# Performance work log

Measured on AMD Instinct MI355X. Metric: run time of the kernel, lower is better.

The kernel has to match this reference:

```python
import jax, jax.numpy as jnp
import numpy as np

N, R, B, H, C, E = 4096, 8, 30, 64, 16, 131072


def setup_inputs() -> dict:
    key = jax.random.key(0)
    ks = jax.random.split(key, 11)
    s = 0.02  # small init scale for weights
    return {
        "x": jax.random.normal(ks[0], (N, N), jnp.float32),
        "edge_index": jax.random.randint(ks[1], (2, E), 0, N, jnp.int32),
        "edge_type": jax.random.randint(ks[2], (E,), 0, R, jnp.int32),
        "basis1": jax.random.normal(ks[3], (B, N, H), jnp.float32) * s,
        "att1": jax.random.normal(ks[4], (R, B), jnp.float32) * s,
        "root1": jax.random.normal(ks[5], (N, H), jnp.float32) * s,
        "bias1": jnp.zeros((H,), jnp.float32),
        "basis2": jax.random.normal(ks[6], (B, H, C), jnp.float32) * s,
        "att2": jax.random.normal(ks[7], (R, B), jnp.float32) * s,
        "root2": jax.random.normal(ks[8], (H, C), jnp.float32) * s,
        "bias2": jnp.zeros((C,), jnp.float32),
    }


def _rgcn_conv(x, src, dst, etype, deg_inv, basis, att, root, bias):
    # Basis-decomposed relation weights: W_r = sum_b att[r,b] * basis[b]
    W = jnp.einsum("rb,bio->rio", att, basis)            # [R, in, out]
    # Pre-transform every node by every relation weight (equivalent to
    # per-edge bmm(x_j, W[edge_type]) but avoids gathering [E, in] features).
    h = jnp.einsum("ni,rio->nro", x, W)                  # [N, R, out]
    msg = h[src, etype]                                  # [E, out] per-edge message
    agg = jax.ops.segment_sum(msg, dst, num_segments=N)  # scatter-add to dst
    agg = agg * deg_inv[:, None]                         # scatter-mean (aggr='mean')
    return agg + x @ root + bias                         # root/self transform + bias


def reference(x, edge_index, edge_type, basis1, att1, root1, bias1,
              basis2, att2, root2, bias2):
    src, dst = edge_index[0], edge_index[1]
    deg = jax.ops.segment_sum(jnp.ones((E,), jnp.float32), dst, num_segments=N)
    deg_inv = 1.0 / jnp.maximum(deg, 1.0)  # zero in-degree -> 0 output, as scatter_mean
    h = jax.nn.relu(_rgcn_conv(x, src, dst, edge_type, deg_inv,
                               basis1, att1, root1, bias1))
    out = _rgcn_conv(h, src, dst, edge_type, deg_inv,
                     basis2, att2, root2, bias2)
    return jax.nn.log_softmax(out, axis=1)
```

## Files before the change

kernel.cpp:

```cpp
#include <hip/hip_runtime.h>
#include <cstdint>

#define E_CNT 131072
#define N_CNT 4096

typedef short bf16x8 __attribute__((ext_vector_type(8)));
typedef float f32x4 __attribute__((ext_vector_type(4)));

__device__ __forceinline__ ushort f2bf(float f) {
  union { float f; unsigned u; } v; v.f = f;
  unsigned r = v.u + 0x7FFFu + ((v.u >> 16) & 1u);
  return (ushort)(r >> 16);
}

__global__ __launch_bounds__(256) void k_zero_deg(int* __restrict__ p) {
  p[blockIdx.x * 256 + threadIdx.x] = 0;
}

__global__ __launch_bounds__(256) void k_prep(const float4* __restrict__ x,
                                              ushort* __restrict__ xbf,
                                              const int* __restrict__ dstp,
                                              int* __restrict__ deg,
                                              const float* __restrict__ att1,
                                              const float* __restrict__ basis1,
                                              float* __restrict__ wtmp,
                                              int* __restrict__ c1i) {
  int bid = blockIdx.x, tid = threadIdx.x;
  if (bid < 16384) {
    int i = bid * 256 + tid;
    float4 v = x[i];
    ushort4 o;
    o.x = f2bf(v.x); o.y = f2bf(v.y); o.z = f2bf(v.z); o.w = f2bf(v.w);
    *(ushort4*)(xbf + (size_t)i * 4) = o;
  } else if (bid < 16896) {
    int e = (bid - 16384) * 256 + tid;
    atomicAdd(&deg[dstp[e]], 1);
  } else if (bid < 17920) {
    int flat = (bid - 16896) * 256 + tid;
    float a[8] = {0.f, 0.f, 0.f, 0.f, 0.f, 0.f, 0.f, 0.f};
    for (int b = 0; b < 30; ++b) {
      float v = basis1[(size_t)b * 262144 + flat];
#pragma unroll
      for (int r = 0; r < 8; ++r) a[r] += att1[r * 30 + b] * v;
    }
#pragma unroll
    for (int r = 0; r < 8; ++r) wtmp[(size_t)r * 262144 + flat] = a[r];
  } else {
    int flat = (bid - 17920) * 256 + tid;
    c1i[flat] = 0;
  }
}

__global__ __launch_bounds__(1024) void k_scan(const int* __restrict__ deg,
                                               int* __restrict__ rowptr,
                                               int* __restrict__ cursor,
                                               float* __restrict__ dinv) {
  __shared__ int part[1024];
  int t = threadIdx.x;
  int base = t * 4;
  int d0 = deg[base], d1 = deg[base + 1], d2 = deg[base + 2], d3 = deg[base + 3];
  int s = d0 + d1 + d2 + d3;
  part[t] = s;
  __syncthreads();
  for (int off = 1; off < 1024; off <<= 1) {
    int v = part[t];
    int u = (t >= off) ? part[t - off] : 0;
    __syncthreads();
    part[t] = v + u;
    __syncthreads();
  }
  int incl = part[t];
  int excl = incl - s;
  int p0 = excl, p1 = excl + d0, p2 = p1 + d1, p3 = p2 + d2;
  rowptr[base] = p0; rowptr[base + 1] = p1; rowptr[base + 2] = p2; rowptr[base + 3] = p3;
  cursor[base] = p0; cursor[base + 1] = p1; cursor[base + 2] = p2; cursor[base + 3] = p3;
  dinv[base]     = 1.0f / fmaxf((float)d0, 1.0f);
  dinv[base + 1] = 1.0f / fmaxf((float)d1, 1.0f);
  dinv[base + 2] = 1.0f / fmaxf((float)d2, 1.0f);
  dinv[base + 3] = 1.0f / fmaxf((float)d3, 1.0f);
  if (t == 1023) rowptr[4096] = incl;
}

__global__ __launch_bounds__(256) void k_mid(const int* __restrict__ srcp,
                                             const int* __restrict__ dstp,
                                             const int* __restrict__ et,
                                             int* __restrict__ cursor,
                                             int* __restrict__ spack,
                                             const float* __restrict__ wtmp,
                                             const float* __restrict__ root1,
                                             ushort* __restrict__ wt1,
                                             const float* __restrict__ att2,
                                             const float* __restrict__ basis2,
                                             const float* __restrict__ root2,
                                             float* __restrict__ w2e) {
  __shared__ float tile[64 * 65];
  int bid = blockIdx.x, t = threadIdx.x;
  if (bid < 512) {
    int e = bid * 256 + t;
    int d = dstp[e];
    int pos = atomicAdd(&cursor[d], 1);
    spack[pos] = (srcp[e] << 3) | et[e];
  } else if (bid < 1088) {
    int bb = bid - 512;
    int r = bb >> 6;
    int i0 = (bb & 63) * 64;
    const float* sp = (r < 8) ? (wtmp + (size_t)r * 262144) : root1;
#pragma unroll
    for (int it = 0; it < 16; ++it) {
      int flat = it * 256 + t;
      int il = flat >> 6, o = flat & 63;
      tile[il * 65 + o] = sp[(size_t)(i0 + il) * 64 + o];
    }
    __syncthreads();
#pragma unroll
    for (int it = 0; it < 16; ++it) {
      int flat = it * 256 + t;
      int o = flat >> 6, il = flat & 63;
      wt1[(size_t)(r * 64 + o) * 4096 + i0 + il] = f2bf(tile[il * 65 + o]);
    }
  } else {
    int r = bid - 1088;
    for (int q = t; q < 1024; q += 256) {
      float a = 0.f;
      if (r < 8) {
        for (int b = 0; b < 30; ++b) a += att2[r * 30 + b] * basis2[b * 1024 + q];
      } else {
        a = root2[q];
      }
      w2e[r * 1024 + q] = a;
    }
  }
}

#define TSTEPS 32
__global__ __launch_bounds__(256) void k_gemm1(const ushort* __restrict__ xbf,
                                               const ushort* __restrict__ wt1,
                                               float* __restrict__ c1) {
  __shared__ __align__(16) ushort As[3][128 * 64];
  __shared__ __align__(16) ushort Bs[3][64 * 64];
  int bid = blockIdx.x;
  int swz = (bid & 7) * 72 + (bid >> 3);
  int kp = swz / 288, t2 = swz % 288;
  int bm = t2 / 9, bn = t2 % 9;
  int m0 = bm * 128, n0 = bn * 64, kbase = kp * 2048;
  int tid = threadIdx.x;
  int lane = tid & 63, wid = tid >> 6;
  int wm = wid >> 1, wn = wid & 1;

  f32x4 acc[4][2] = {};

  auto stage = [&](int s, int k0) {
#pragma unroll
    for (int it = 0; it < 4; ++it) {
      int flat = it * 256 + tid;
      int row = flat >> 3, gg = flat & 7;
      int gcol = k0 + ((gg ^ (row & 7)) << 3);
      const ushort* g = xbf + (size_t)(m0 + row) * 4096 + gcol;
      ushort* l = &As[s][(it * 256 + wid * 64) * 8];
      __builtin_amdgcn_global_load_lds((const __attribute__((address_space(1))) void*)g,
                                       (__attribute__((address_space(3))) void*)l, 16, 0, 0);
    }
#pragma unroll
    for (int it = 0; it < 2; ++it) {
      int flat = it * 256 + tid;
      int row = flat >> 3, gg = flat & 7;
      int gcol = k0 + ((gg ^ (row & 7)) << 3);
      const ushort* g = wt1 + (size_t)(n0 + row) * 4096 + gcol;
      ushort* l = &Bs[s][(it * 256 + wid * 64) * 8];
      __builtin_amdgcn_global_load_lds((const __attribute__((address_space(1))) void*)g,
                                       (__attribute__((address_space(3))) void*)l, 16, 0, 0);
    }
  };

  stage(0, kbase);
  stage(1, kbase + 64);

  int cb = 0;
  for (int t = 0; t < TSTEPS; ++t) {
    if (t < TSTEPS - 1) {
      asm volatile("s_waitcnt vmcnt(6)" ::: "memory");
    } else {
      asm volatile("s_waitcnt vmcnt(0)" ::: "memory");
    }
    __builtin_amdgcn_s_barrier();
    if (t + 2 < TSTEPS) {
      int sb = cb == 0 ? 2 : cb - 1;
      stage(sb, kbase + (t + 2) * 64);
    }
    int q = lane >> 4, sw = lane & 7, r16 = lane & 15;
    bf16x8 a[2][4], b[2][2];
#pragma unroll
    for (int ks = 0; ks < 2; ++ks) {
      int co = ((ks * 4 + q) ^ sw) << 3;
#pragma unroll
      for (int ni = 0; ni < 2; ++ni)
        b[ks][ni] = *(const bf16x8*)&Bs[cb][(wn * 32 + ni * 16 + r16) * 64 + co];
#pragma unroll
      for (int mi = 0; mi < 4; ++mi)
        a[ks][mi] = *(const bf16x8*)&As[cb][(wm * 64 + mi * 16 + r16) * 64 + co];
    }
    __builtin_amdgcn_s_setprio(1);
#pragma unroll
    for (int ks = 0; ks < 2; ++ks)
#pragma unroll
      for (int mi = 0; mi < 4; ++mi)
#pragma unroll
        for (int ni = 0; ni < 2; ++ni)
          acc[mi][ni] = __builtin_amdgcn_mfma_f32_16x16x32_bf16(a[ks][mi], b[ks][ni], acc[mi][ni], 0, 0, 0);
    __builtin_amdgcn_s_setprio(0);
    cb = cb == 2 ? 0 : cb + 1;
  }

  int cf = lane & 15, rf4 = (lane >> 4) * 4;
#pragma unroll
  for (int mi = 0; mi < 4; ++mi)
#pragma unroll
    for (int ni = 0; ni < 2; ++ni) {
      int gcol = n0 + wn * 32 + ni * 16 + cf;
#pragma unroll
      for (int j = 0; j < 4; ++j) {
        int grow = m0 + wm * 64 + mi * 16 + rf4 + j;
        atomicAdd(&c1[(size_t)grow * 576 + gcol], acc[mi][ni][j]);
      }
    }
}

__global__ __launch_bounds__(256) void k_agg1h2(const float* __restrict__ c1,
                                                const int* __restrict__ rowptr,
                                                const int* __restrict__ spack,
                                                const float* __restrict__ dinv,
                                                const float* __restrict__ bias1,
                                                const float* __restrict__ w2e,
                                                float* __restrict__ h2c) {
  __shared__ float sh[4][64];
  int g = threadIdx.x >> 6, t = threadIdx.x & 63;
  int n = blockIdx.x * 4 + g;
  int s0 = rowptr[n], s1 = rowptr[n + 1];
  float acc = 0.f;
  int e = s0;
  for (; e + 3 < s1; e += 4) {
    int p0 = spack[e], p1 = spack[e + 1], p2 = spack[e + 2], p3 = spack[e + 3];
    float v0 = c1[(size_t)(p0 >> 3) * 576 + (p0 & 7) * 64 + t];
    float v1 = c1[(size_t)(p1 >> 3) * 576 + (p1 & 7) * 64 + t];
    float v2 = c1[(size_t)(p2 >> 3) * 576 + (p2 & 7) * 64 + t];
    float v3 = c1[(size_t)(p3 >> 3) * 576 + (p3 & 7) * 64 + t];
    acc += (v0 + v1) + (v2 + v3);
  }
  for (; e < s1; ++e) {
    int p = spack[e];
    acc += c1[(size_t)(p >> 3) * 576 + (p & 7) * 64 + t];
  }
  float v = acc * dinv[n] + c1[(size_t)n * 576 + 512 + t] + bias1[t];
  sh[g][t] = fmaxf(v, 0.f);
  __syncthreads();
  float* o = h2c + (size_t)n * 144;
  for (int rc = t; rc < 144; rc += 64) {
    int r9 = rc >> 4, c = rc & 15;
    const float* w = w2e + r9 * 1024 + c;
    float a = 0.f;
#pragma unroll
    for (int hh = 0; hh < 64; ++hh) a += sh[g][hh] * w[hh * 16];
    o[rc] = a;
  }
}

__global__ __launch_bounds__(64) void k_agg2(const float* __restrict__ h2c,
                                             const int* __restrict__ rowptr,
                                             const int* __restrict__ spack,
                                             const float* __restrict__ dinv,
                                             const float* __restrict__ bias2,
                                             float* __restrict__ out) {
  __shared__ float red[64];
  int n = blockIdx.x, t = threadIdx.x;
  int c = t & 15, q = t >> 4;
  int s0 = rowptr[n], s1 = rowptr[n + 1];
  float acc = 0.f;
  for (int e = s0 + q; e < s1; e += 4) {
    int p = spack[e];
    acc += h2c[(size_t)(p >> 3) * 144 + (p & 7) * 16 + c];
  }
  red[t] = acc;
  __syncthreads();
  if (t < 16) {
    float sum = red[c] + red[16 + c] + red[32 + c] + red[48 + c];
    float v = sum * dinv[n] + h2c[(size_t)n * 144 + 128 + c] + bias2[c];
    float m = v;
#pragma unroll
    for (int off = 1; off < 16; off <<= 1) m = fmaxf(m, __shfl_xor(m, off, 64));
    float ex = expf(v - m);
    float s = ex;
#pragma unroll
    for (int off = 1; off < 16; off <<= 1) s += __shfl_xor(s, off, 64);
    out[n * 16 + c] = v - m - logf(s);
  }
}

extern "C" void kernel_launch(void* const* d_in, const int* in_sizes, int n_in,
                              void* d_out, int out_size, void* d_ws, size_t ws_size,
                              hipStream_t stream) {
  const float* x      = (const float*)d_in[0];
  const int*   ei     = (const int*)d_in[1];
  const int*   et     = (const int*)d_in[2];
  const float* basis1 = (const float*)d_in[3];
  const float* att1   = (const float*)d_in[4];
  const float* root1  = (const float*)d_in[5];
  const float* bias1  = (const float*)d_in[6];
  const float* basis2 = (const float*)d_in[7];
  const float* att2   = (const float*)d_in[8];
  const float* root2  = (const float*)d_in[9];
  const float* bias2  = (const float*)d_in[10];
  float* out = (float*)d_out;

  char* ws = (char*)d_ws;
  size_t off = 0;
  auto alloc = [&](size_t bytes) {
    void* p = ws + off;
    off = (off + bytes + 255) & ~(size_t)255;
    return p;
  };
  ushort* xbf  = (ushort*)alloc((size_t)N_CNT * N_CNT * 2);
  ushort* wt1  = (ushort*)alloc((size_t)576 * 4096 * 2);
  float*  wtmp = (float*)alloc((size_t)8 * N_CNT * 64 * 4);
  float*  c1   = (float*)alloc((size_t)N_CNT * 576 * 4);
  float*  w2e  = (float*)alloc((size_t)9 * 64 * 16 * 4);
  float*  h2c  = (float*)alloc((size_t)N_CNT * 144 * 4);
  int*    deg    = (int*)alloc(4096 * 4);
  float*  dinv   = (float*)alloc(4096 * 4);
  int*    rowptr = (int*)alloc(4097 * 4);
  int*    cursor = (int*)alloc(4096 * 4);
  int*    spack  = (int*)alloc((size_t)E_CNT * 4);

  const int* srcp = ei;
  const int* dstp = ei + E_CNT;

  k_zero_deg<<<16, 256, 0, stream>>>(deg);
  k_prep<<<27136, 256, 0, stream>>>((const float4*)x, xbf, dstp, deg,
                                    att1, basis1, wtmp, (int*)c1);
  k_scan<<<1, 1024, 0, stream>>>(deg, rowptr, cursor, dinv);
  k_mid<<<1097, 256, 0, stream>>>(srcp, dstp, et, cursor, spack,
                                  wtmp, root1, wt1, att2, basis2, root2, w2e);
  k_gemm1<<<576, 256, 0, stream>>>(xbf, wt1, c1);
  k_agg1h2<<<1024, 256, 0, stream>>>(c1, rowptr, spack, dinv, bias1, w2e, h2c);
  k_agg2<<<4096, 64, 0, stream>>>(h2c, rowptr, spack, dinv, bias2, out);
}
```

Before: 142.0 us.

## Fuse basis combine with bf16 transpose and split GEMM K into more blocks

The relation-weight combination now writes transposed bf16 weights straight into wt1 inside the prep kernel, which removes the fp32 wtmp intermediate and the transpose pass in k_mid. The degree zeroing moves to a hipMemsetAsync. The first GEMM drops its triple-buffered LDS pipeline for a single-buffered loop with barriers, halves the K range per block, and doubles the grid to 1152 blocks with a higher occupancy hint. This trades overlap of loads and compute for more resident blocks, and it doubles the atomicAdd traffic into c1.

```diff
diff --git a/kernel.cpp b/kernel.cpp
--- a/kernel.cpp
+++ b/kernel.cpp
@@ -11,10 +11,6 @@
   union { float f; unsigned u; } v; v.f = f;
   unsigned r = v.u + 0x7FFFu + ((v.u >> 16) & 1u);
   return (ushort)(r >> 16);
-}
-
-__global__ __launch_bounds__(256) void k_zero_deg(int* __restrict__ p) {
-  p[blockIdx.x * 256 + threadIdx.x] = 0;
 }
 
 __global__ __launch_bounds__(256) void k_prep(const float4* __restrict__ x,
@@ -23,30 +19,71 @@
                                               int* __restrict__ deg,
                                               const float* __restrict__ att1,
                                               const float* __restrict__ basis1,
-                                              float* __restrict__ wtmp,
+                                              const float* __restrict__ root1,
+                                              ushort* __restrict__ wt1,
                                               int* __restrict__ c1i) {
-  int bid = blockIdx.x, tid = threadIdx.x;
+  __shared__ float sT[32 * 33];
+  int bid = blockIdx.x, t = threadIdx.x;
   if (bid < 16384) {
-    int i = bid * 256 + tid;
+    int i = bid * 256 + t;
     float4 v = x[i];
     ushort4 o;
     o.x = f2bf(v.x); o.y = f2bf(v.y); o.z = f2bf(v.z); o.w = f2bf(v.w);
     *(ushort4*)(xbf + (size_t)i * 4) = o;
   } else if (bid < 16896) {
-    int e = (bid - 16384) * 256 + tid;
+    int e = (bid - 16384) * 256 + t;
     atomicAdd(&deg[dstp[e]], 1);
-  } else if (bid < 17920) {
-    int flat = (bid - 16896) * 256 + tid;
-    float a[8] = {0.f, 0.f, 0.f, 0.f, 0.f, 0.f, 0.f, 0.f};
+  } else if (bid < 17152) {
+    int bb = bid - 16896;
+    int i0 = (bb >> 1) * 32, o0 = (bb & 1) * 32;
+    int ol = t & 31, ir = t >> 5;
+    float a[8][4] = {};
     for (int b = 0; b < 30; ++b) {
-      float v = basis1[(size_t)b * 262144 + flat];
-#pragma unroll
-      for (int r = 0; r < 8; ++r) a[r] += att1[r * 30 + b] * v;
-    }
-#pragma unroll
-    for (int r = 0; r < 8; ++r) wtmp[(size_t)r * 262144 + flat] = a[r];
+      float w0 = att1[0 * 30 + b], w1 = att1[1 * 30 + b], w2 = att1[2 * 30 + b], w3 = att1[3 * 30 + b];
+      float w4 = att1[4 * 30 + b], w5 = att1[5 * 30 + b], w6 = att1[6 * 30 + b], w7 = att1[7 * 30 + b];
+#pragma unroll
+      for (int k = 0; k < 4; ++k) {
+        float v = basis1[(size_t)b * 262144 + (size_t)(i0 + ir + k * 8) * 64 + o0 + ol];
+        a[0][k] += w0 * v; a[1][k] += w1 * v; a[2][k] += w2 * v; a[3][k] += w3 * v;
+        a[4][k] += w4 * v; a[5][k] += w5 * v; a[6][k] += w6 * v; a[7][k] += w7 * v;
+      }
+    }
+    for (int r = 0; r < 8; ++r) {
+#pragma unroll
+      for (int k = 0; k < 4; ++k) sT[ol * 33 + ir + k * 8] = a[r][k];
+      __syncthreads();
+#pragma unroll
+      for (int k = 0; k < 4; ++k) {
+        int orow = ir + k * 8, icol = ol;
+        wt1[(size_t)(r * 64 + o0 + orow) * 4096 + i0 + icol] = f2bf(sT[orow * 33 + icol]);
+      }
+      __syncthreads();
+    }
+  } else if (bid < 17168) {
+    int bb = bid - 17152;
+    int i0 = bb * 256;
+    int ol = t & 31, ir = t >> 5;
+    for (int s = 0; s < 8; ++s) {
+      int ib = i0 + s * 32;
+#pragma unroll
+      for (int k = 0; k < 4; ++k) {
+      }
+      for (int oh = 0; oh < 2; ++oh) {
+        int o0 = oh * 32;
+#pragma unroll
+        for (int k = 0; k < 4; ++k)
+          sT[ol * 33 + ir + k * 8] = root1[(size_t)(ib + ir + k * 8) * 64 + o0 + ol];
+        __syncthreads();
+#pragma unroll
+        for (int k = 0; k < 4; ++k) {
+          int orow = ir + k * 8, icol = ol;
+          wt1[(size_t)(512 + o0 + orow) * 4096 + ib + icol] = f2bf(sT[orow * 33 + icol]);
+        }
+        __syncthreads();
+      }
+    }
   } else {
-    int flat = (bid - 17920) * 256 + tid;
+    int flat = (bid - 17168) * 256 + t;
     c1i[flat] = 0;
   }
 }
@@ -86,40 +123,18 @@
                                              const int* __restrict__ et,
                                              int* __restrict__ cursor,
                                              int* __restrict__ spack,
-                                             const float* __restrict__ wtmp,
-                                             const float* __restrict__ root1,
-                                             ushort* __restrict__ wt1,
                                              const float* __restrict__ att2,
                                              const float* __restrict__ basis2,
                                              const float* __restrict__ root2,
                                              float* __restrict__ w2e) {
-  __shared__ float tile[64 * 65];
   int bid = blockIdx.x, t = threadIdx.x;
   if (bid < 512) {
     int e = bid * 256 + t;
     int d = dstp[e];
     int pos = atomicAdd(&cursor[d], 1);
     spack[pos] = (srcp[e] << 3) | et[e];
-  } else if (bid < 1088) {
-    int bb = bid - 512;
-    int r = bb >> 6;
-    int i0 = (bb & 63) * 64;
-    const float* sp = (r < 8) ? (wtmp + (size_t)r * 262144) : root1;
-#pragma unroll
-    for (int it = 0; it < 16; ++it) {
-      int flat = it * 256 + t;
-      int il = flat >> 6, o = flat & 63;
-      tile[il * 65 + o] = sp[(size_t)(i0 + il) * 64 + o];
-    }
-    __syncthreads();
-#pragma unroll
-    for (int it = 0; it < 16; ++it) {
-      int flat = it * 256 + t;
-      int o = flat >> 6, il = flat & 63;
-      wt1[(size_t)(r * 64 + o) * 4096 + i0 + il] = f2bf(tile[il * 65 + o]);
-    }
   } else {
-    int r = bid - 1088;
+    int r = bid - 512;
     for (int q = t; q < 1024; q += 256) {
       float a = 0.f;
       if (r < 8) {
@@ -132,31 +147,31 @@
   }
 }
 
-#define TSTEPS 32
-__global__ __launch_bounds__(256) void k_gemm1(const ushort* __restrict__ xbf,
-                                               const ushort* __restrict__ wt1,
-                                               float* __restrict__ c1) {
-  __shared__ __align__(16) ushort As[3][128 * 64];
-  __shared__ __align__(16) ushort Bs[3][64 * 64];
+__global__ __launch_bounds__(256, 5) void k_gemm1(const ushort* __restrict__ xbf,
+                                                  const ushort* __restrict__ wt1,
+                                                  float* __restrict__ c1) {
+  __shared__ __align__(16) ushort As[128 * 64];
+  __shared__ __align__(16) ushort Bs[64 * 64];
   int bid = blockIdx.x;
-  int swz = (bid & 7) * 72 + (bid >> 3);
+  int swz = (bid & 7) * 144 + (bid >> 3);
   int kp = swz / 288, t2 = swz % 288;
   int bm = t2 / 9, bn = t2 % 9;
-  int m0 = bm * 128, n0 = bn * 64, kbase = kp * 2048;
+  int m0 = bm * 128, n0 = bn * 64, kbase = kp * 1024;
   int tid = threadIdx.x;
   int lane = tid & 63, wid = tid >> 6;
   int wm = wid >> 1, wn = wid & 1;
 
   f32x4 acc[4][2] = {};
 
-  auto stage = [&](int s, int k0) {
+  for (int tt = 0; tt < 16; ++tt) {
+    int k0 = kbase + tt * 64;
 #pragma unroll
     for (int it = 0; it < 4; ++it) {
       int flat = it * 256 + tid;
       int row = flat >> 3, gg = flat & 7;
       int gcol = k0 + ((gg ^ (row & 7)) << 3);
       const ushort* g = xbf + (size_t)(m0 + row) * 4096 + gcol;
-      ushort* l = &As[s][(it * 256 + wid * 64) * 8];
+      ushort* l = &As[(it * 256 + wid * 64) * 8];
       __builtin_amdgcn_global_load_lds((const __attribute__((address_space(1))) void*)g,
                                        (__attribute__((address_space(3))) void*)l, 16, 0, 0);
     }
@@ -166,49 +181,33 @@
       int row = flat >> 3, gg = flat & 7;
       int gcol = k0 + ((gg ^ (row & 7)) << 3);
       const ushort* g = wt1 + (size_t)(n0 + row) * 4096 + gcol;
-      ushort* l = &Bs[s][(it * 256 + wid * 64) * 8];
+      ushort* l = &Bs[(it * 256 + wid * 64) * 8];
       __builtin_amdgcn_global_load_lds((const __attribute__((address_space(1))) void*)g,
                                        (__attribute__((address_space(3))) void*)l, 16, 0, 0);
     }
-  };
-
-  stage(0, kbase);
-  stage(1, kbase + 64);
-
-  int cb = 0;
-  for (int t = 0; t < TSTEPS; ++t) {
-    if (t < TSTEPS - 1) {
-      asm volatile("s_waitcnt vmcnt(6)" ::: "memory");
-    } else {
-      asm volatile("s_waitcnt vmcnt(0)" ::: "memory");
-    }
-    __builtin_amdgcn_s_barrier();
-    if (t + 2 < TSTEPS) {
-      int sb = cb == 0 ? 2 : cb - 1;
-      stage(sb, kbase + (t + 2) * 64);
-    }
+    __syncthreads();
     int q = lane >> 4, sw = lane & 7, r16 = lane & 15;
-    bf16x8 a[2][4], b[2][2];
 #pragma unroll
     for (int ks = 0; ks < 2; ++ks) {
       int co = ((ks * 4 + q) ^ sw) << 3;
-#pragma unroll
-      for (int ni = 0; ni < 2; ++ni)
-        b[ks][ni] = *(const bf16x8*)&Bs[cb][(wn * 32 + ni * 16 + r16) * 64 + co];
-#pragma unroll
-      for (int mi = 0; mi < 4; ++mi)
-        a[ks][mi] = *(const bf16x8*)&As[cb][(wm * 64 + mi * 16 + r16) * 64 + co];
-    }
-    __builtin_amdgcn_s_setprio(1);
-#pragma unroll
-    for (int ks = 0; ks < 2; ++ks)
-#pragma unroll
-      for (int mi = 0; mi < 4; ++mi)
-#pragma unroll
-        for (int ni = 0; ni < 2; ++ni)
-          acc[mi][ni] = __builtin_amdgcn_mfma_f32_16x16x32_bf16(a[ks][mi], b[ks][ni], acc[mi][ni], 0, 0, 0);
-    __builtin_amdgcn_s_setprio(0);
-    cb = cb == 2 ? 0 : cb + 1;
+      bf16x8 b0 = *(const bf16x8*)&Bs[(wn * 32 + 0 * 16 + r16) * 64 + co];
+      bf16x8 b1 = *(const bf16x8*)&Bs[(wn * 32 + 1 * 16 + r16) * 64 + co];
+      bf16x8 a0 = *(const bf16x8*)&As[(wm * 64 + 0 * 16 + r16) * 64 + co];
+      bf16x8 a1 = *(const bf16x8*)&As[(wm * 64 + 1 * 16 + r16) * 64 + co];
+      bf16x8 a2 = *(const bf16x8*)&As[(wm * 64 + 2 * 16 + r16) * 64 + co];
+      bf16x8 a3 = *(const bf16x8*)&As[(wm * 64 + 3 * 16 + r16) * 64 + co];
+      __builtin_amdgcn_s_setprio(1);
+      acc[0][0] = __builtin_amdgcn_mfma_f32_16x16x32_bf16(a0, b0, acc[0][0], 0, 0, 0);
+      acc[0][1] = __builtin_amdgcn_mfma_f32_16x16x32_bf16(a0, b1, acc[0][1], 0, 0, 0);
+      acc[1][0] = __builtin_amdgcn_mfma_f32_16x16x32_bf16(a1, b0, acc[1][0], 0, 0, 0);
+      acc[1][1] = __builtin_amdgcn_mfma_f32_16x16x32_bf16(a1, b1, acc[1][1], 0, 0, 0);
+      acc[2][0] = __builtin_amdgcn_mfma_f32_16x16x32_bf16(a2, b0, acc[2][0], 0, 0, 0);
+      acc[2][1] = __builtin_amdgcn_mfma_f32_16x16x32_bf16(a2, b1, acc[2][1], 0, 0, 0);
+      acc[3][0] = __builtin_amdgcn_mfma_f32_16x16x32_bf16(a3, b0, acc[3][0], 0, 0, 0);
+      acc[3][1] = __builtin_amdgcn_mfma_f32_16x16x32_bf16(a3, b1, acc[3][1], 0, 0, 0);
+      __builtin_amdgcn_s_setprio(0);
+    }
+    __syncthreads();
   }
 
   int cf = lane & 15, rf4 = (lane >> 4) * 4;
@@ -320,7 +319,6 @@
   };
   ushort* xbf  = (ushort*)alloc((size_t)N_CNT * N_CNT * 2);
   ushort* wt1  = (ushort*)alloc((size_t)576 * 4096 * 2);
-  float*  wtmp = (float*)alloc((size_t)8 * N_CNT * 64 * 4);
   float*  c1   = (float*)alloc((size_t)N_CNT * 576 * 4);
   float*  w2e  = (float*)alloc((size_t)9 * 64 * 16 * 4);
   float*  h2c  = (float*)alloc((size_t)N_CNT * 144 * 4);
@@ -333,13 +331,13 @@
   const int* srcp = ei;
   const int* dstp = ei + E_CNT;
 
-  k_zero_deg<<<16, 256, 0, stream>>>(deg);
-  k_prep<<<27136, 256, 0, stream>>>((const float4*)x, xbf, dstp, deg,
-                                    att1, basis1, wtmp, (int*)c1);
+  hipMemsetAsync(deg, 0, 4096 * 4, stream);
+  k_prep<<<26384, 256, 0, stream>>>((const float4*)x, xbf, dstp, deg,
+                                    att1, basis1, root1, wt1, (int*)c1);
   k_scan<<<1, 1024, 0, stream>>>(deg, rowptr, cursor, dinv);
-  k_mid<<<1097, 256, 0, stream>>>(srcp, dstp, et, cursor, spack,
-                                  wtmp, root1, wt1, att2, basis2, root2, w2e);
-  k_gemm1<<<576, 256, 0, stream>>>(xbf, wt1, c1);
+  k_mid<<<521, 256, 0, stream>>>(srcp, dstp, et, cursor, spack,
+                                 att2, basis2, root2, w2e);
+  k_gemm1<<<1152, 256, 0, stream>>>(xbf, wt1, c1);
   k_agg1h2<<<1024, 256, 0, stream>>>(c1, rowptr, spack, dinv, bias1, w2e, h2c);
   k_agg2<<<4096, 64, 0, stream>>>(h2c, rowptr, spack, dinv, bias2, out);
 }
```

After: 131.4 us. 7.5% less time.
